# Kernel optimization log

Measured on AMD Instinct MI355X. Metric: run time of the kernel, lower is better.

The kernel has to match this reference:

```python
import jax, jax.numpy as jnp
import numpy as np


def setup_inputs() -> dict:
    key = jax.random.key(0)
    k1, k2, k3, k4 = jax.random.split(key, 4)
    B, S, D = 4, 2048, 1024
    scale = 1.0 / np.sqrt(D)
    x = jax.random.normal(k1, (B, S, D), dtype=jnp.float32)
    Wq = jax.random.normal(k2, (D, D), dtype=jnp.float32) * scale
    Wk = jax.random.normal(k3, (D, D), dtype=jnp.float32) * scale
    Wv = jax.random.normal(k4, (D, D), dtype=jnp.float32) * scale
    return {"x": x, "Wq": Wq, "Wk": Wk, "Wv": Wv}


def reference(x, Wq, Wk, Wv):
    # x: [B, S, D]; Wq/Wk/Wv: [d_out, d_in] torch Linear convention (y = x @ W.T)
    B, S, D = x.shape
    q = jnp.einsum('bsd,od->bso', x, Wq)
    k = jnp.einsum('bsd,od->bso', x, Wk)
    v = jnp.einsum('bsd,od->bso', x, Wv)
    scores = jnp.einsum('bqo,bko->bqk', q, k)  # [B, S, S]
    causal = jnp.tril(jnp.ones((S, S), dtype=bool))  # True = keep
    scores = jnp.where(causal, scores, -jnp.inf)
    d_out = q.shape[-1]
    attn = jax.nn.softmax(scores / jnp.sqrt(jnp.asarray(d_out, x.dtype)), axis=-1)
    # dropout_prob = 0.0 -> identity
    return jnp.einsum('bqk,bko->bqo', attn, v)
```

## Files before the change

### kernel.cpp

```cpp
#include <hip/hip_runtime.h>
#include <hip/hip_bf16.h>
#include <stdint.h>

typedef __attribute__((ext_vector_type(8))) short bf16x8;
typedef __attribute__((ext_vector_type(4))) float f32x4;

__device__ __forceinline__ float bf2f(unsigned short u) {
    union { unsigned int i; float f; } z; z.i = ((unsigned int)u) << 16; return z.f;
}
__device__ __forceinline__ unsigned short f2bf(float f) {
    union { float f; unsigned int i; } z; z.f = f;
    unsigned int x = z.i;
    unsigned int r = x + 0x7fffu + ((x >> 16) & 1u);
    return (unsigned short)(r >> 16);
}

typedef const __attribute__((address_space(1))) unsigned int* gp_t;
typedef __attribute__((address_space(3))) unsigned int* lp_t;

__device__ __forceinline__ void gload_lds16(const void* g, void* l) {
    __builtin_amdgcn_global_load_lds((gp_t)g, (lp_t)l, 16, 0, 0);
}

__device__ __forceinline__ int xcd_remap(int orig, int nwg) {
    const int q = nwg >> 3, r = nwg & 7;
    const int xcd = orig & 7, pos = orig >> 3;
    return (xcd < r ? xcd * (q + 1) : r * (q + 1) + (xcd - r) * q) + pos;
}

__global__ __launch_bounds__(256) void cvt_xv(const float* __restrict__ x,
                                              const float* __restrict__ wv,
                                              unsigned short* __restrict__ xb,
                                              unsigned short* __restrict__ wvb) {
    const int NX = 1 << 21;
    const int DD4 = 1 << 18;
    const int total = NX + DD4;
    int i = blockIdx.x * 256 + threadIdx.x;
    const int stride = gridDim.x * 256;
    for (; i < total; i += stride) {
        float4 v = (i < NX) ? reinterpret_cast<const float4*>(x)[i]
                            : reinterpret_cast<const float4*>(wv)[i - NX];
        ushort4 u;
        u.x = f2bf(v.x); u.y = f2bf(v.y); u.z = f2bf(v.z); u.w = f2bf(v.w);
        if (i < NX) reinterpret_cast<ushort4*>(xb)[i] = u;
        else        reinterpret_cast<ushort4*>(wvb)[i - NX] = u;
    }
}

__global__ __launch_bounds__(256) void tr_w(const float* __restrict__ wq,
                                            const float* __restrict__ wk,
                                            unsigned short* __restrict__ wqT,
                                            unsigned short* __restrict__ wkT) {
    const int id = blockIdx.x;
    const int m = id >> 8;
    const int t = id & 255;
    const int tr = t >> 4, tc = t & 15;
    const float* src = m ? wk : wq;
    unsigned short* dst = m ? wkT : wqT;
    const float scale = m ? 1.0f : 0.03125f;

    __shared__ unsigned short tile[64][65];
    const int tid = threadIdx.x;
    const int r0 = tid >> 4;
    const int c4 = tid & 15;
    #pragma unroll
    for (int p = 0; p < 4; ++p) {
        const int r = p * 16 + r0;
        float4 v = reinterpret_cast<const float4*>(
            src + (size_t)(tr * 64 + r) * 1024 + tc * 64)[c4];
        tile[c4 * 4 + 0][r] = f2bf(v.x * scale);
        tile[c4 * 4 + 1][r] = f2bf(v.y * scale);
        tile[c4 * 4 + 2][r] = f2bf(v.z * scale);
        tile[c4 * 4 + 3][r] = f2bf(v.w * scale);
    }
    __syncthreads();
    const int cr = tid >> 2;
    const int q4 = tid & 3;
    #pragma unroll
    for (int p = 0; p < 4; ++p) {
        const int off = (q4 * 4 + p) * 4;
        ushort4 u;
        u.x = tile[cr][off + 0]; u.y = tile[cr][off + 1];
        u.z = tile[cr][off + 2]; u.w = tile[cr][off + 3];
        *reinterpret_cast<ushort4*>(dst + (size_t)(tc * 64 + cr) * 1024 + tr * 64 + off) = u;
    }
}

#define MFMA(a, b, c) __builtin_amdgcn_mfma_f32_16x16x32_bf16(a, b, c, 0, 0, 0)
#define SB() __builtin_amdgcn_sched_barrier(0)
#define BAR() __builtin_amdgcn_s_barrier()
#define LGKM0() asm volatile("s_waitcnt lgkmcnt(0)" ::: "memory")

__device__ __forceinline__ void gemm256_core(
    const unsigned short* __restrict__ Ab,
    const unsigned short* __restrict__ Bb,
    int m0, int n0,
    unsigned short (&As)[2][256 * 64], unsigned short (&Bs)[2][256 * 64],
    f32x4 (&acc)[8][4])
{
    constexpr int LD = 1024, NK = 16;
    const int tid = threadIdx.x;
    const int l = tid & 63, w = tid >> 6;
    const int wr = w >> 2, wc = w & 3;

    const int srow = w * 8 + (l >> 3);
    const int scol = ((l & 7) ^ (l >> 3)) * 8;
    const size_t ldst = (size_t)w * 1024 + (size_t)l * 16;

    auto stageA = [&](int t, int h, int b) {
        const unsigned short* src = Ab + (size_t)(m0 + h * 128 + srow) * LD + t * 64 + scol;
        char* dst = (char*)&As[b][0] + h * 16384 + ldst;
        gload_lds16(src, dst);
        gload_lds16(src + (size_t)64 * LD, dst + 8192);
    };
    auto stageB = [&](int t, int h, int b) {
        const unsigned short* src = Bb + (size_t)(n0 + h * 128 + srow) * LD + t * 64 + scol;
        char* dst = (char*)&Bs[b][0] + h * 16384 + ldst;
        gload_lds16(src, dst);
        gload_lds16(src + (size_t)64 * LD, dst + 8192);
    };

    const int l15 = l & 15, l7 = l & 7;
    const int s0 = (((l >> 4) ^ l7) * 16);
    const int s1 = ((((l >> 4) + 4) ^ l7) * 16);

    bf16x8 Af[4][2], Bf0[2][2], Bf1[2][2];

    stageA(0, 0, 0); stageA(0, 1, 0); stageB(0, 0, 0); stageB(0, 1, 0);
    stageB(1, 0, 1); stageB(1, 1, 1);
    asm volatile("s_waitcnt vmcnt(4)" ::: "memory");
    SB(); BAR(); SB();

    for (int t = 0; t < NK; ++t) {
        const int b = t & 1, bn = b ^ 1;
        const char* ab = (const char*)&As[b][0] + (wr * 128 + l15) * 128;
        const char* bb = (const char*)&Bs[b][0] + (wc * 64 + l15) * 128;

        #pragma unroll
        for (int mi = 0; mi < 4; ++mi) {
            Af[mi][0] = *(const bf16x8*)(ab + mi * 2048 + s0);
            Af[mi][1] = *(const bf16x8*)(ab + mi * 2048 + s1);
        }
        #pragma unroll
        for (int ni = 0; ni < 2; ++ni) {
            Bf0[ni][0] = *(const bf16x8*)(bb + ni * 2048 + s0);
            Bf0[ni][1] = *(const bf16x8*)(bb + ni * 2048 + s1);
        }
        if (t + 1 < NK) stageA(t + 1, 0, bn);
        BAR(); LGKM0(); SB();
        __builtin_amdgcn_s_setprio(1);
        #pragma unroll
        for (int mi = 0; mi < 4; ++mi)
            #pragma unroll
            for (int ni = 0; ni < 2; ++ni) {
                acc[mi][ni] = MFMA(Af[mi][0], Bf0[ni][0], acc[mi][ni]);
                acc[mi][ni] = MFMA(Af[mi][1], Bf0[ni][1], acc[mi][ni]);
            }
        __builtin_amdgcn_s_setprio(0);
        SB(); BAR(); SB();

        #pragma unroll
        for (int ni = 0; ni < 2; ++ni) {
            Bf1[ni][0] = *(const bf16x8*)(bb + 4096 + ni * 2048 + s0);
            Bf1[ni][1] = *(const bf16x8*)(bb + 4096 + ni * 2048 + s1);
        }
        if (t + 1 < NK) stageA(t + 1, 1, bn);
        BAR(); LGKM0(); SB();
        __builtin_amdgcn_s_setprio(1);
        #pragma unroll
        for (int mi = 0; mi < 4; ++mi)
            #pragma unroll
            for (int ni = 0; ni < 2; ++ni) {
                acc[mi][2 + ni] = MFMA(Af[mi][0], Bf1[ni][0], acc[mi][2 + ni]);
                acc[mi][2 + ni] = MFMA(Af[mi][1], Bf1[ni][1], acc[mi][2 + ni]);
            }
        __builtin_amdgcn_s_setprio(0);
        SB(); BAR(); SB();

        #pragma unroll
        for (int mi = 0; mi < 4; ++mi) {
            Af[mi][0] = *(const bf16x8*)(ab + 8192 + mi * 2048 + s0);
            Af[mi][1] = *(const bf16x8*)(ab + 8192 + mi * 2048 + s1);
        }
        if (t + 2 < NK) stageB(t + 2, 0, b);
        BAR(); LGKM0(); SB();
        __builtin_amdgcn_s_setprio(1);
        #pragma unroll
        for (int mi = 0; mi < 4; ++mi)
            #pragma unroll
            for (int ni = 0; ni < 2; ++ni) {
                acc[4 + mi][2 + ni] = MFMA(Af[mi][0], Bf1[ni][0], acc[4 + mi][2 + ni]);
                acc[4 + mi][2 + ni] = MFMA(Af[mi][1], Bf1[ni][1], acc[4 + mi][2 + ni]);
            }
        __builtin_amdgcn_s_setprio(0);
        SB(); BAR(); SB();

        if (t + 2 < NK) stageB(t + 2, 1, b);
        BAR(); SB();
        __builtin_amdgcn_s_setprio(1);
        #pragma unroll
        for (int mi = 0; mi < 4; ++mi)
            #pragma unroll
            for (int ni = 0; ni < 2; ++ni) {
                acc[4 + mi][ni] = MFMA(Af[mi][0], Bf0[ni][0], acc[4 + mi][ni]);
                acc[4 + mi][ni] = MFMA(Af[mi][1], Bf0[ni][1], acc[4 + mi][ni]);
            }
        __builtin_amdgcn_s_setprio(0);
        if (t + 2 < NK) {
            asm volatile("s_waitcnt vmcnt(4)" ::: "memory");
        } else if (t + 1 < NK) {
            asm volatile("s_waitcnt vmcnt(0)" ::: "memory");
        }
        SB(); BAR(); SB();
    }
}

__global__ __launch_bounds__(512, 2) void tv_proj(
    const unsigned short* __restrict__ xb, const unsigned short* __restrict__ wst,
    const unsigned short* __restrict__ wvb,
    unsigned short* __restrict__ tb, unsigned short* __restrict__ vt)
{
    const int wg = xcd_remap(blockIdx.x, 256);

    __shared__ unsigned short As[2][256 * 64];
    __shared__ unsigned short Bs[2][256 * 64];
    f32x4 acc[8][4] = {};

    const int tid = threadIdx.x;
    const int l = tid & 63, w = tid >> 6;
    const int wr = w >> 2, wc = w & 3;
    const int crow = (l >> 4) * 4, ccol = l & 15;

    if (wg < 128) {
        const int mt = wg & 31, nt = wg >> 5;
        const int m0 = mt * 256, n0 = nt * 256;
        gemm256_core(xb, wst, m0, n0, As, Bs, acc);
        #pragma unroll
        for (int mi = 0; mi < 8; ++mi)
            #pragma unroll
            for (int ni = 0; ni < 4; ++ni) {
                const size_t rbase = (size_t)(m0 + wr * 128 + mi * 16 + crow);
                const size_t cg = (size_t)(n0 + wc * 64 + ni * 16 + ccol);
                #pragma unroll
                for (int r = 0; r < 4; ++r)
                    tb[(rbase + r) * 1024 + cg] = f2bf(acc[mi][ni][r]);
            }
    } else {
        const int v = wg - 128;
        const int mt = v & 31, nt = v >> 5;
        const int m0 = mt * 256, n0 = nt * 256;
        gemm256_core(xb, wvb, m0, n0, As, Bs, acc);
        #pragma unroll
        for (int mi = 0; mi < 8; ++mi)
            #pragma unroll
            for (int ni = 0; ni < 4; ++ni) {
                const int rbase = m0 + wr * 128 + mi * 16 + crow;
                const int o = n0 + wc * 64 + ni * 16 + ccol;
                ushort4 u;
                u.x = f2bf(acc[mi][ni][0]);
                u.y = f2bf(acc[mi][ni][1]);
                u.z = f2bf(acc[mi][ni][2]);
                u.w = f2bf(acc[mi][ni][3]);
                *reinterpret_cast<ushort4*>(&vt[(size_t)o * 8192 + rbase]) = u;
            }
    }
}

__device__ __forceinline__ void gemm128_core64(
    const unsigned short* __restrict__ Ab, int lda,
    const unsigned short* __restrict__ Bb, int ldb,
    int m0, int n0, int nk,
    unsigned short (&As)[2][128 * 64], unsigned short (&Bs)[2][128 * 64],
    f32x4 (&acc)[4][4])
{
    const int tid = threadIdx.x;
    const int l = tid & 63, w = tid >> 6;
    const int wr = w >> 1, wc = w & 1;
    const int l15 = l & 15;

    const int srow = w * 8 + (l >> 3);
    const int scol = ((l & 7) ^ (l >> 3)) * 8;
    const size_t ldst = (size_t)w * 1024 + (size_t)l * 16;

    auto stage = [&](int t, int b) {
        const int k0 = t * 64;
        #pragma unroll
        for (int i = 0; i < 4; ++i) {
            gload_lds16(Ab + (size_t)(m0 + i * 32 + srow) * lda + k0 + scol,
                        (char*)&As[b][0] + i * 4096 + ldst);
            gload_lds16(Bb + (size_t)(n0 + i * 32 + srow) * ldb + k0 + scol,
                        (char*)&Bs[b][0] + i * 4096 + ldst);
        }
    };

    const int s0 = (((l >> 4) ^ (l & 7)) * 16);
    const int s1 = ((((l >> 4) + 4) ^ (l & 7)) * 16);

    stage(0, 0);
    if (nk > 1) {
        stage(1, 1);
        asm volatile("s_waitcnt vmcnt(8)" ::: "memory");
    } else {
        asm volatile("s_waitcnt vmcnt(0)" ::: "memory");
    }
    SB(); BAR(); SB();

    for (int t = 0; t < nk; ++t) {
        const int b = t & 1;
        const char* ab = (const char*)&As[b][0] + (wr * 64 + l15) * 128;
        const char* bb = (const char*)&Bs[b][0] + (wc * 64 + l15) * 128;
        bf16x8 af[4][2], bfr[4][2];
        #pragma unroll
        for (int m = 0; m < 4; ++m) {
            af[m][0] = *(const bf16x8*)(ab + m * 2048 + s0);
            af[m][1] = *(const bf16x8*)(ab + m * 2048 + s1);
        }
        #pragma unroll
        for (int n = 0; n < 4; ++n) {
            bfr[n][0] = *(const bf16x8*)(bb + n * 2048 + s0);
            bfr[n][1] = *(const bf16x8*)(bb + n * 2048 + s1);
        }
        LGKM0(); SB();
        BAR(); SB();
        if (t + 2 < nk) stage(t + 2, b);

        __builtin_amdgcn_s_setprio(1);
        #pragma unroll
        for (int m = 0; m < 4; ++m)
            #pragma unroll
            for (int n = 0; n < 4; ++n) {
                acc[m][n] = MFMA(af[m][0], bfr[n][0], acc[m][n]);
                acc[m][n] = MFMA(af[m][1], bfr[n][1], acc[m][n]);
            }
        __builtin_amdgcn_s_setprio(0);

        if (t + 2 < nk) {
            asm volatile("s_waitcnt vmcnt(8)" ::: "memory");
        } else if (t + 1 < nk) {
            asm volatile("s_waitcnt vmcnt(0)" ::: "memory");
        }
        SB(); BAR(); SB();
    }
}

__global__ __launch_bounds__(256) void wst128(
    const unsigned short* __restrict__ wkT, const unsigned short* __restrict__ wqT,
    unsigned short* __restrict__ wst)
{
    const int wg = xcd_remap(blockIdx.x, 64);
    const int mt = wg & 7, nt = wg >> 3;
    const int m0 = mt * 128, n0 = nt * 128;

    __shared__ unsigned short As[2][128 * 64];
    __shared__ unsigned short Bs[2][128 * 64];
    f32x4 acc[4][4] = {};

    gemm128_core64(wkT, 1024, wqT, 1024, m0, n0, 16, As, Bs, acc);

    const int tid = threadIdx.x;
    const int l = tid & 63, w = tid >> 6;
    const int wr = w >> 1, wc = w & 1;
    const int crow = (l >> 4) * 4, ccol = l & 15;
    #pragma unroll
    for (int m = 0; m < 4; ++m)
        #pragma unroll
        for (int n = 0; n < 4; ++n) {
            const size_t rbase = (size_t)(m0 + wr * 64 + m * 16 + crow);
            const size_t cg = (size_t)(n0 + wc * 64 + n * 16 + ccol);
            #pragma unroll
            for (int r = 0; r < 4; ++r)
                wst[(rbase + r) * 1024 + cg] = f2bf(acc[m][n][r]);
        }
}

__global__ __launch_bounds__(256) void scores128(
    const unsigned short* __restrict__ tb, const unsigned short* __restrict__ xb,
    unsigned short* __restrict__ sc)
{
    const int wg = xcd_remap(blockIdx.x, 544);

    __shared__ unsigned short As[2][128 * 64];
    __shared__ unsigned short Bs[2][128 * 64];
    f32x4 acc[4][4] = {};

    const int z = wg / 136, r = wg % 136;
    int mt = (int)((__builtin_sqrtf(8.f * r + 1.f) - 1.f) * 0.5f);
    while ((mt + 1) * (mt + 2) / 2 <= r) ++mt;
    while (mt * (mt + 1) / 2 > r) --mt;
    const int nt = r - mt * (mt + 1) / 2;
    const int m0 = mt * 128, n0 = nt * 128;
    const unsigned short* Ab = tb + (size_t)z * 2048 * 1024;
    const unsigned short* Bb = xb + (size_t)z * 2048 * 1024;
    gemm128_core64(Ab, 1024, Bb, 1024, m0, n0, 16, As, Bs, acc);

    const int tid = threadIdx.x;
    const int l = tid & 63, w = tid >> 6;
    const int wr = w >> 1, wc = w & 1;
    const int crow = (l >> 4) * 4, ccol = l & 15;
    unsigned short* C = sc + (size_t)z * 2048 * 2048;
    #pragma unroll
    for (int m = 0; m < 4; ++m)
        #pragma unroll
        for (int n = 0; n < 4; ++n) {
            const size_t rbase = (size_t)(m0 + wr * 64 + m * 16 + crow);
            const size_t cg = (size_t)(n0 + wc * 64 + n * 16 + ccol);
            #pragma unroll
            for (int r2 = 0; r2 < 4; ++r2)
                C[(rbase + r2) * 2048 + cg] = f2bf(acc[m][n][r2]);
        }
}

__global__ __launch_bounds__(256) void gemm128_pv(
    const unsigned short* __restrict__ A, int lda, long long sA,
    const unsigned short* __restrict__ B, int ldb, long long sB,
    float* __restrict__ C, int ldc, long long sC, int K)
{
    const int orig = blockIdx.x;
    const int h = orig >> 8;
    const int c = xcd_remap(orig & 255, 256);
    const int z = c >> 6;
    const int rem = c & 63;
    const int nt = rem >> 3;
    const int j = rem & 7;
    const int mt = h ? (15 - j) : j;

    const unsigned short* Ab = A + (size_t)z * sA;
    const unsigned short* Bb = B + (size_t)z * sB;
    const int Keff = ((mt + 1) * 128 < K) ? (mt + 1) * 128 : K;
    const int nk = Keff >> 6;

    __shared__ unsigned short As[2][128 * 64];
    __shared__ unsigned short Bs[2][128 * 64];
    f32x4 acc[4][4] = {};

    gemm128_core64(Ab, lda, Bb, ldb, mt * 128, nt * 128, nk, As, Bs, acc);

    const int tid = threadIdx.x;
    const int l = tid & 63, w = tid >> 6;
    const int wr = w >> 1, wc = w & 1;
    const int crow = (l >> 4) * 4, ccol = l & 15;
    float* Cb = C + (size_t)z * sC;
    #pragma unroll
    for (int m = 0; m < 4; ++m)
        #pragma unroll
        for (int n = 0; n < 4; ++n) {
            const size_t rbase = (size_t)(mt * 128 + wr * 64 + m * 16 + crow);
            const size_t cg = (size_t)(nt * 128 + wc * 64 + n * 16 + ccol);
            #pragma unroll
            for (int r = 0; r < 4; ++r)
                Cb[(rbase + r) * ldc + cg] = acc[m][n][r];
        }
}

__global__ __launch_bounds__(256) void softmax_causal(unsigned short* __restrict__ P) {
    const int S = 2048;
    const int w = threadIdx.x >> 6, l = threadIdx.x & 63;
    const int gq = blockIdx.x * 4 + w;
    const int q = gq & (S - 1);
    unsigned short* row = P + (size_t)gq * S;
    const int wlim = ((q >> 7) + 1) << 7;
    const float NEG = -__builtin_huge_valf();

    float f[4][8];
    #pragma unroll
    for (int p = 0; p < 4; ++p) {
        const int c0 = p * 512 + l * 8;
        if (p * 512 <= q && c0 <= q) {
            uint4 rv = *reinterpret_cast<const uint4*>(row + c0);
            unsigned short us[8];
            us[0] = rv.x & 0xffff; us[1] = rv.x >> 16;
            us[2] = rv.y & 0xffff; us[3] = rv.y >> 16;
            us[4] = rv.z & 0xffff; us[5] = rv.z >> 16;
            us[6] = rv.w & 0xffff; us[7] = rv.w >> 16;
            #pragma unroll
            for (int i = 0; i < 8; ++i)
                f[p][i] = (c0 + i <= q) ? bf2f(us[i]) : NEG;
        } else {
            #pragma unroll
            for (int i = 0; i < 8; ++i) f[p][i] = NEG;
        }
    }

    float m = NEG;
    #pragma unroll
    for (int p = 0; p < 4; ++p)
        #pragma unroll
        for (int i = 0; i < 8; ++i) m = fmaxf(m, f[p][i]);
    #pragma unroll
    for (int o = 1; o < 64; o <<= 1) m = fmaxf(m, __shfl_xor(m, o));

    float s = 0.f;
    #pragma unroll
    for (int p = 0; p < 4; ++p)
        #pragma unroll
        for (int i = 0; i < 8; ++i) {
            f[p][i] = exp2f((f[p][i] - m) * 1.44269504f);
            s += f[p][i];
        }
    #pragma unroll
    for (int o = 1; o < 64; o <<= 1) s += __shfl_xor(s, o);
    const float inv = 1.0f / s;

    #pragma unroll
    for (int p = 0; p < 4; ++p) {
        const int c0 = p * 512 + l * 8;
        if (p * 512 < wlim && c0 < wlim) {
            uint4 ov;
            ov.x = f2bf(f[p][0] * inv) | ((unsigned int)f2bf(f[p][1] * inv) << 16);
            ov.y = f2bf(f[p][2] * inv) | ((unsigned int)f2bf(f[p][3] * inv) << 16);
            ov.z = f2bf(f[p][4] * inv) | ((unsigned int)f2bf(f[p][5] * inv) << 16);
            ov.w = f2bf(f[p][6] * inv) | ((unsigned int)f2bf(f[p][7] * inv) << 16);
            *reinterpret_cast<uint4*>(row + c0) = ov;
        }
    }
}

extern "C" void kernel_launch(void* const* d_in, const int* in_sizes, int n_in,
                              void* d_out, int out_size, void* d_ws, size_t ws_size,
                              hipStream_t stream) {
    const float* x  = (const float*)d_in[0];
    const float* Wq = (const float*)d_in[1];
    const float* Wk = (const float*)d_in[2];
    const float* Wv = (const float*)d_in[3];
    float* out = (float*)d_out;

    const int S = 2048;

    char* ws = (char*)d_ws;
    unsigned short* xb  = (unsigned short*)(ws);
    unsigned short* wvb = (unsigned short*)(ws + (16ull << 20));
    unsigned short* wqT = (unsigned short*)(ws + (18ull << 20));
    unsigned short* wkT = (unsigned short*)(ws + (20ull << 20));
    unsigned short* wst = (unsigned short*)(ws + (22ull << 20));
    unsigned short* tb  = (unsigned short*)(ws + (24ull << 20));
    unsigned short* vt  = (unsigned short*)(ws + (40ull << 20));
    unsigned short* sc  = (unsigned short*)(ws + (56ull << 20));

    cvt_xv<<<2048, 256, 0, stream>>>(x, Wv, xb, wvb);
    tr_w<<<512, 256, 0, stream>>>(Wq, Wk, wqT, wkT);

    wst128<<<64, 256, 0, stream>>>(wkT, wqT, wst);

    tv_proj<<<256, 512, 0, stream>>>(xb, wst, wvb, tb, vt);

    scores128<<<544, 256, 0, stream>>>(tb, xb, sc);

    softmax_causal<<<2048, 256, 0, stream>>>(sc);

    gemm128_pv<<<512, 256, 0, stream>>>(
        sc, S, (long long)S * S, vt, 8192, S, out, 1024, (long long)S * 1024, S);
}
```

Before: 144.8 us.

## Fuse conversion kernels, interleave T/V projection roles, compute V^T as Wv·x^T

Merges the x/Wv bf16 conversion and the Wq/Wk transpose into one launch to drop a kernel launch and its tail. In the projection kernel, T and V blocks are interleaved per XCD by slot parity instead of XCD-remapped contiguous ranges. The V^T tile is now computed directly by swapping operands (Wv as A, x as B), so stores run along rows instead of as a strided transposed write. The cost is scalar 2-byte stores in the V epilogue and a different L2 locality pattern.

```diff
diff --git a/kernel.cpp b/kernel.cpp
--- a/kernel.cpp
+++ b/kernel.cpp
@@ -28,61 +28,60 @@
     return (xcd < r ? xcd * (q + 1) : r * (q + 1) + (xcd - r) * q) + pos;
 }
 
-__global__ __launch_bounds__(256) void cvt_xv(const float* __restrict__ x,
-                                              const float* __restrict__ wv,
-                                              unsigned short* __restrict__ xb,
-                                              unsigned short* __restrict__ wvb) {
-    const int NX = 1 << 21;
-    const int DD4 = 1 << 18;
-    const int total = NX + DD4;
-    int i = blockIdx.x * 256 + threadIdx.x;
-    const int stride = gridDim.x * 256;
-    for (; i < total; i += stride) {
-        float4 v = (i < NX) ? reinterpret_cast<const float4*>(x)[i]
-                            : reinterpret_cast<const float4*>(wv)[i - NX];
-        ushort4 u;
-        u.x = f2bf(v.x); u.y = f2bf(v.y); u.z = f2bf(v.z); u.w = f2bf(v.w);
-        if (i < NX) reinterpret_cast<ushort4*>(xb)[i] = u;
-        else        reinterpret_cast<ushort4*>(wvb)[i - NX] = u;
-    }
-}
-
-__global__ __launch_bounds__(256) void tr_w(const float* __restrict__ wq,
-                                            const float* __restrict__ wk,
-                                            unsigned short* __restrict__ wqT,
-                                            unsigned short* __restrict__ wkT) {
+__global__ __launch_bounds__(256) void cvt_tr(
+    const float* __restrict__ x, const float* __restrict__ wq,
+    const float* __restrict__ wk, const float* __restrict__ wv,
+    unsigned short* __restrict__ xb, unsigned short* __restrict__ wvb,
+    unsigned short* __restrict__ wqT, unsigned short* __restrict__ wkT) {
     const int id = blockIdx.x;
-    const int m = id >> 8;
-    const int t = id & 255;
-    const int tr = t >> 4, tc = t & 15;
-    const float* src = m ? wk : wq;
-    unsigned short* dst = m ? wkT : wqT;
-    const float scale = m ? 1.0f : 0.03125f;
-
-    __shared__ unsigned short tile[64][65];
-    const int tid = threadIdx.x;
-    const int r0 = tid >> 4;
-    const int c4 = tid & 15;
-    #pragma unroll
-    for (int p = 0; p < 4; ++p) {
-        const int r = p * 16 + r0;
-        float4 v = reinterpret_cast<const float4*>(
-            src + (size_t)(tr * 64 + r) * 1024 + tc * 64)[c4];
-        tile[c4 * 4 + 0][r] = f2bf(v.x * scale);
-        tile[c4 * 4 + 1][r] = f2bf(v.y * scale);
-        tile[c4 * 4 + 2][r] = f2bf(v.z * scale);
-        tile[c4 * 4 + 3][r] = f2bf(v.w * scale);
-    }
-    __syncthreads();
-    const int cr = tid >> 2;
-    const int q4 = tid & 3;
-    #pragma unroll
-    for (int p = 0; p < 4; ++p) {
-        const int off = (q4 * 4 + p) * 4;
-        ushort4 u;
-        u.x = tile[cr][off + 0]; u.y = tile[cr][off + 1];
-        u.z = tile[cr][off + 2]; u.w = tile[cr][off + 3];
-        *reinterpret_cast<ushort4*>(dst + (size_t)(tc * 64 + cr) * 1024 + tr * 64 + off) = u;
+    if (id < 2048) {
+        const int NX = 1 << 21;
+        const int DD4 = 1 << 18;
+        const int total = NX + DD4;
+        int i = id * 256 + threadIdx.x;
+        const int stride = 2048 * 256;
+        for (; i < total; i += stride) {
+            float4 v = (i < NX) ? reinterpret_cast<const float4*>(x)[i]
+                                : reinterpret_cast<const float4*>(wv)[i - NX];
+            ushort4 u;
+            u.x = f2bf(v.x); u.y = f2bf(v.y); u.z = f2bf(v.z); u.w = f2bf(v.w);
+            if (i < NX) reinterpret_cast<ushort4*>(xb)[i] = u;
+            else        reinterpret_cast<ushort4*>(wvb)[i - NX] = u;
+        }
+    } else {
+        const int id2 = id - 2048;
+        const int m = id2 >> 8;
+        const int t = id2 & 255;
+        const int tr = t >> 4, tc = t & 15;
+        const float* src = m ? wk : wq;
+        unsigned short* dst = m ? wkT : wqT;
+        const float scale = m ? 1.0f : 0.03125f;
+
+        __shared__ unsigned short tile[64][65];
+        const int tid = threadIdx.x;
+        const int r0 = tid >> 4;
+        const int c4 = tid & 15;
+        #pragma unroll
+        for (int p = 0; p < 4; ++p) {
+            const int r = p * 16 + r0;
+            float4 v = reinterpret_cast<const float4*>(
+                src + (size_t)(tr * 64 + r) * 1024 + tc * 64)[c4];
+            tile[c4 * 4 + 0][r] = f2bf(v.x * scale);
+            tile[c4 * 4 + 1][r] = f2bf(v.y * scale);
+            tile[c4 * 4 + 2][r] = f2bf(v.z * scale);
+            tile[c4 * 4 + 3][r] = f2bf(v.w * scale);
+        }
+        __syncthreads();
+        const int cr = tid >> 2;
+        const int q4 = tid & 3;
+        #pragma unroll
+        for (int p = 0; p < 4; ++p) {
+            const int off = (q4 * 4 + p) * 4;
+            ushort4 u;
+            u.x = tile[cr][off + 0]; u.y = tile[cr][off + 1];
+            u.z = tile[cr][off + 2]; u.w = tile[cr][off + 3];
+            *reinterpret_cast<ushort4*>(dst + (size_t)(tc * 64 + cr) * 1024 + tr * 64 + off) = u;
+        }
     }
 }
 
@@ -220,7 +219,10 @@
     const unsigned short* __restrict__ wvb,
     unsigned short* __restrict__ tb, unsigned short* __restrict__ vt)
 {
-    const int wg = xcd_remap(blockIdx.x, 256);
+    const int j = blockIdx.x;
+    const int xcd = j & 7, slot = j >> 3;
+    const int role = slot & 1;
+    const int id_r = xcd * 16 + (slot >> 1);
 
     __shared__ unsigned short As[2][256 * 64];
     __shared__ unsigned short Bs[2][256 * 64];
@@ -231,8 +233,8 @@
     const int wr = w >> 2, wc = w & 3;
     const int crow = (l >> 4) * 4, ccol = l & 15;
 
-    if (wg < 128) {
-        const int mt = wg & 31, nt = wg >> 5;
+    if (role == 0) {
+        const int mt = id_r & 31, nt = id_r >> 5;
         const int m0 = mt * 256, n0 = nt * 256;
         gemm256_core(xb, wst, m0, n0, As, Bs, acc);
         #pragma unroll
@@ -246,22 +248,18 @@
                     tb[(rbase + r) * 1024 + cg] = f2bf(acc[mi][ni][r]);
             }
     } else {
-        const int v = wg - 128;
-        const int mt = v & 31, nt = v >> 5;
+        const int mt = id_r & 3, nt = id_r >> 2;
         const int m0 = mt * 256, n0 = nt * 256;
-        gemm256_core(xb, wvb, m0, n0, As, Bs, acc);
+        gemm256_core(wvb, xb, m0, n0, As, Bs, acc);
         #pragma unroll
         for (int mi = 0; mi < 8; ++mi)
             #pragma unroll
             for (int ni = 0; ni < 4; ++ni) {
-                const int rbase = m0 + wr * 128 + mi * 16 + crow;
-                const int o = n0 + wc * 64 + ni * 16 + ccol;
-                ushort4 u;
-                u.x = f2bf(acc[mi][ni][0]);
-                u.y = f2bf(acc[mi][ni][1]);
-                u.z = f2bf(acc[mi][ni][2]);
-                u.w = f2bf(acc[mi][ni][3]);
-                *reinterpret_cast<ushort4*>(&vt[(size_t)o * 8192 + rbase]) = u;
+                const size_t rbase = (size_t)(m0 + wr * 128 + mi * 16 + crow);
+                const size_t cg = (size_t)(n0 + wc * 64 + ni * 16 + ccol);
+                #pragma unroll
+                for (int r = 0; r < 4; ++r)
+                    vt[(rbase + r) * 8192 + cg] = f2bf(acc[mi][ni][r]);
             }
     }
 }
@@ -536,8 +534,7 @@
     unsigned short* vt  = (unsigned short*)(ws + (40ull << 20));
     unsigned short* sc  = (unsigned short*)(ws + (56ull << 20));
 
-    cvt_xv<<<2048, 256, 0, stream>>>(x, Wv, xb, wvb);
-    tr_w<<<512, 256, 0, stream>>>(Wq, Wk, wqT, wkT);
+    cvt_tr<<<2560, 256, 0, stream>>>(x, Wq, Wk, Wv, xb, wvb, wqT, wkT);
 
     wst128<<<64, 256, 0, stream>>>(wkT, wqT, wst);
 
```

New measurement: 137.8 us, median of 2. 1.05x faster.
